# Kernel tuning notes

Measured on AMD Instinct MI355X. Metric: run time of the kernel, lower is better.

## Reference

```python
import jax, jax.numpy as jnp
import numpy as np

N = 200000
E = 6400000


def setup_inputs() -> dict:
    key = jax.random.key(0)
    k1, k2, k3, k4 = jax.random.split(key, 4)
    x = jax.random.normal(k1, (N, 10), dtype=jnp.float32)
    edge_index = jax.random.randint(k2, (2, E), 0, N, dtype=jnp.int64)
    W1 = jax.random.normal(k3, (10, 16), dtype=jnp.float32) * (1.0 / np.sqrt(10))
    b1 = jnp.zeros((16,), dtype=jnp.float32)
    W2 = jax.random.normal(k4, (16, 2), dtype=jnp.float32) * (1.0 / np.sqrt(16))
    b2 = jnp.zeros((2,), dtype=jnp.float32)
    return {"x": x, "edge_index": edge_index, "W1": W1, "b1": b1, "W2": W2, "b2": b2}


def gcn_layer(x, src, dst, W, b, num_nodes):
    # GCNConv: out = D^{-1/2} (A + I) D^{-1/2} (x W) + b, deg computed on A+I
    loop = jnp.arange(num_nodes, dtype=src.dtype)
    s = jnp.concatenate([src, loop])
    d = jnp.concatenate([dst, loop])
    deg = jax.ops.segment_sum(jnp.ones(s.shape[0], dtype=x.dtype), d, num_segments=num_nodes)
    dinv = jnp.where(deg > 0, jax.lax.rsqrt(deg), 0.0)
    norm = dinv[s] * dinv[d]                      # [E+N]
    h = x @ W                                     # [N, out] (transform before gather)
    msg = h[s] * norm[:, None]                    # [E+N, out]
    return jax.ops.segment_sum(msg, d, num_segments=num_nodes) + b


def reference(x, edge_index, W1, b1, W2, b2):
    src, dst = edge_index[0], edge_index[1]
    n = x.shape[0]
    h = jax.nn.relu(gcn_layer(x, src, dst, W1, b1, n))
    return gcn_layer(h, src, dst, W2, b2, n)
```

## Files before the change

### kernel.cpp

```cpp
#include <hip/hip_runtime.h>
#include <hip/hip_fp16.h>

#define BLK 256
#define BBLK 512
#define ABLK 512
#define DBLK 512
#define NBK 782
#define BW 256
#define CAP 8960
#define NCH 3
#define CHUNK 6144


__global__ void k_hist(const int* __restrict__ dst, int e, int* __restrict__ gcnt,
                       int* __restrict__ blockhist) {
  __shared__ int h[NBK];
  for (int i = threadIdx.x; i < NBK; i += BLK) h[i] = 0;
  __syncthreads();
  int base = blockIdx.x * CHUNK;
  int m = min(CHUNK, e - base);
  for (int k = threadIdx.x; k < m; k += BLK) atomicAdd(&h[dst[base + k] >> 8], 1);
  __syncthreads();
  int* row = blockhist + (size_t)blockIdx.x * NBK;
  int sft = (blockIdx.x * 193) % NBK;
  for (int bb = threadIdx.x; bb < NBK; bb += BLK) {
    int b = bb + sft; if (b >= NBK) b -= NBK;
    int c = h[b];
    row[b] = c;
    if (c) atomicAdd(&gcnt[b], c);
  }
}

__global__ void k_scan(const int* __restrict__ gcnt, int* __restrict__ gbase,
                       int* __restrict__ gcur, int e) {
  __shared__ int s[1024];
  int t = threadIdx.x;
  int v = (t < NBK) ? gcnt[t] : 0;
  s[t] = v;
  __syncthreads();
  for (int d = 1; d < 1024; d <<= 1) {
    int u = (t >= d) ? s[t - d] : 0;
    __syncthreads();
    s[t] += u;
    __syncthreads();
  }
  if (t < NBK) { int ex = s[t] - v; gbase[t] = ex; gcur[t] = ex; }
  if (t == 0) gbase[NBK] = e;
}

__global__ void __launch_bounds__(BBLK) k_bin(const int* __restrict__ src,
                                              const int* __restrict__ dst, int e,
                                              int* __restrict__ gcur,
                                              const int* __restrict__ blockhist,
                                              unsigned* __restrict__ binned) {
  __shared__ int lcnt[NBK];
  __shared__ int loff[NBK + 1];
  __shared__ int lbase[NBK];
  __shared__ int part[BBLK];
  __shared__ unsigned sorted[CHUNK];
  __shared__ unsigned short bkt16[CHUNK];
  int t = threadIdx.x;
  int base = blockIdx.x * CHUNK;
  int m = min(CHUNK, e - base);

  const int* row = blockhist + (size_t)blockIdx.x * NBK;
  for (int i = t; i < NBK; i += BBLK) lcnt[i] = row[i];
  __syncthreads();
  int b0 = 2 * t;
  int s0 = (b0 + 0 < NBK) ? lcnt[b0 + 0] : 0;
  int s1 = (b0 + 1 < NBK) ? lcnt[b0 + 1] : 0;
  int tsum = s0 + s1;
  part[t] = tsum;
  __syncthreads();
  for (int d = 1; d < BBLK; d <<= 1) {
    int u = (t >= d) ? part[t - d] : 0;
    __syncthreads();
    part[t] += u;
    __syncthreads();
  }
  int ex = part[t] - tsum;
  if (b0 + 0 < NBK) loff[b0 + 0] = ex;
  if (b0 + 1 < NBK) loff[b0 + 1] = ex + s0;
  if (t == 0) loff[NBK] = m;
  __syncthreads();
  int sft = (blockIdx.x * 193) % NBK;
  for (int bb = t; bb < NBK; bb += BBLK) {
    int b = bb + sft; if (b >= NBK) b -= NBK;
    int c = lcnt[b];
    lbase[b] = c ? atomicAdd(&gcur[b], c) : 0;
  }
  __syncthreads();
  for (int b = t; b < NBK; b += BBLK) lcnt[b] = loff[b];
  __syncthreads();
  for (int k = t; k < m; k += BBLK) {
    int d = dst[base + k];
    int b = d >> 8;
    int dl = d & 255;
    int pos = atomicAdd(&lcnt[b], 1);
    sorted[pos] = (unsigned)src[base + k] | ((unsigned)dl << 18);
    bkt16[pos] = (unsigned short)b;
  }
  __syncthreads();
  for (int i = t; i < m; i += BBLK) {
    int b = bkt16[i];
    binned[lbase[b] + (i - loff[b])] = sorted[i];
  }
}

__global__ void __launch_bounds__(DBLK) k_ldeg_t1(const unsigned* __restrict__ binned,
                                                  const int* __restrict__ gbase,
                                                  const float* __restrict__ x,
                                                  const float* __restrict__ W1,
                                                  int* __restrict__ deg,
                                                  float* __restrict__ dinv,
                                                  __half* __restrict__ hs1, int n) {
  __shared__ int cnt[2][BW];
  __shared__ float w[160];
  int t = threadIdx.x;
  cnt[t >> 8][t & 255] = 0;
  if (t < 160) w[t] = W1[t];
  __syncthreads();
  int b = blockIdx.x;
  int p0 = gbase[b], p1 = gbase[b + 1];
  int h = t >> 8;
  for (int p = p0 + t; p < p1; p += DBLK) atomicAdd(&cnt[h][binned[p] >> 18], 1);
  __syncthreads();
  if (t >= BW) return;
  int v = b * BW + t;
  int dg = cnt[0][t] + cnt[1][t];
  deg[v] = dg;
  if (v >= n) return;
  float di = rsqrtf((float)dg + 1.0f);
  dinv[v] = di;
  float xi[10];
#pragma unroll
  for (int k = 0; k < 10; k++) xi[k] = x[(size_t)v * 10 + k];
  __half2 hv[8];
#pragma unroll
  for (int j = 0; j < 8; j++) {
    float acc0 = 0.f, acc1 = 0.f;
#pragma unroll
    for (int k = 0; k < 10; k++) {
      acc0 = fmaf(xi[k], w[k * 16 + 2 * j], acc0);
      acc1 = fmaf(xi[k], w[k * 16 + 2 * j + 1], acc1);
    }
    hv[j] = __floats2half2_rn(acc0 * di, acc1 * di);
  }
  float4* o = (float4*)(hs1 + (size_t)v * 16);
  o[0] = *(float4*)&hv[0];
  o[1] = *(float4*)&hv[4];
}

__global__ void __launch_bounds__(ABLK) k_agg1s(unsigned* __restrict__ binned,
                                                const int* __restrict__ gbase,
                                                const int* __restrict__ deg,
                                                int* __restrict__ doff,
                                                const __half* __restrict__ hs1,
                                                const float* __restrict__ dinv,
                                                const float* __restrict__ b1,
                                                const float* __restrict__ W2,
                                                float* __restrict__ hs2, int n) {
  __shared__ int cnt[BW];
  __shared__ int stmp[BW];
  __shared__ int off[BW + 1];
  __shared__ int cur[BW];
  __shared__ int sorted[CAP];
  __shared__ float w2[32];
  __shared__ float sb1[16];
  int t = threadIdx.x;
  if (t < 32) w2[t] = W2[t];
  if (t >= 32 && t < 48) sb1[t - 32] = b1[t - 32];
  int bkt = blockIdx.x;
  int p0 = gbase[bkt], p1 = gbase[bkt + 1];
  const bool fast = (p1 - p0) <= CAP;
  const int j = t >> 1;
  const int c = t & 1;
  float acc[8];
#pragma unroll
  for (int q = 0; q < 8; q++) acc[q] = 0.f;

#define ACCR(R) { const __half2* h2_ = (const __half2*)&R; \
    float2 f0_ = __half22float2(h2_[0]); \
    float2 f1_ = __half22float2(h2_[1]); \
    float2 f2_ = __half22float2(h2_[2]); \
    float2 f3_ = __half22float2(h2_[3]); \
    acc[0] += f0_.x; acc[1] += f0_.y; acc[2] += f1_.x; acc[3] += f1_.y; \
    acc[4] += f2_.x; acc[5] += f2_.y; acc[6] += f3_.x; acc[7] += f3_.y; }

  int p = p0;
  int cidx = 0;
  while (p < p1) {
    int m = min(CAP, p1 - p);
    if (fast) {
      if (t < BW) cnt[t] = deg[(bkt << 8) + t];
    } else {
      if (t < BW) cnt[t] = 0;
      __syncthreads();
      for (int i = t; i < m; i += ABLK) atomicAdd(&cnt[binned[p + i] >> 18], 1);
    }
    __syncthreads();
    if (t < BW) stmp[t] = cnt[t];
    __syncthreads();
    for (int d = 1; d < BW; d <<= 1) {
      int u = 0;
      if (t < BW && t >= d) u = stmp[t - d];
      __syncthreads();
      if (t < BW) stmp[t] += u;
      __syncthreads();
    }
    if (t < BW) { int ex = stmp[t] - cnt[t]; off[t] = ex; cur[t] = ex; }
    if (t == 0) off[BW] = m;
    __syncthreads();
    for (int i = t; i < m; i += ABLK) {
      unsigned pk = binned[p + i];
      int pos = atomicAdd(&cur[pk >> 18], 1);
      sorted[pos] = (int)(pk & 0x3FFFF);
    }
    __syncthreads();
    for (int i = t; i < m; i += ABLK) binned[p + i] = (unsigned)sorted[i];
    if (cidx < NCH && t <= BW) doff[((size_t)bkt * NCH + cidx) * (BW + 1) + t] = off[t];
    int i0 = off[j], i1 = off[j + 1];
    int i = i0;
    for (; i + 3 < i1; i += 4) {
      int s0 = sorted[i + 0];
      int s1 = sorted[i + 1];
      int s2 = sorted[i + 2];
      int s3 = sorted[i + 3];
      float4 r0 = *(const float4*)(hs1 + (size_t)s0 * 16 + c * 8);
      float4 r1 = *(const float4*)(hs1 + (size_t)s1 * 16 + c * 8);
      float4 r2 = *(const float4*)(hs1 + (size_t)s2 * 16 + c * 8);
      float4 r3 = *(const float4*)(hs1 + (size_t)s3 * 16 + c * 8);
      ACCR(r0); ACCR(r1); ACCR(r2); ACCR(r3);
    }
    for (; i < i1; i++) {
      int s = sorted[i];
      float4 r = *(const float4*)(hs1 + (size_t)s * 16 + c * 8);
      ACCR(r);
    }
    __syncthreads();
    p += m;
    cidx++;
  }
#undef ACCR

  int v = bkt * BW + j;
  if (v < n) {
    float di = dinv[v];
    float4 sf = *(const float4*)(hs1 + (size_t)v * 16 + c * 8);
    const __half2* sh = (const __half2*)&sf;
    float h0c = 0.f, h1c = 0.f;
#pragma unroll
    for (int q = 0; q < 4; q++) {
      float2 sv = __half22float2(sh[q]);
      int f0 = c * 8 + 2 * q;
      int f1 = f0 + 1;
      float a0 = fmaxf(fmaf(di, acc[2 * q + 0] + sv.x, sb1[f0]), 0.f);
      float a1 = fmaxf(fmaf(di, acc[2 * q + 1] + sv.y, sb1[f1]), 0.f);
      h0c = fmaf(a0, w2[f0 * 2 + 0], fmaf(a1, w2[f1 * 2 + 0], h0c));
      h1c = fmaf(a0, w2[f0 * 2 + 1], fmaf(a1, w2[f1 * 2 + 1], h1c));
    }
    float h0 = h0c + __shfl_xor(h0c, 1);
    float h1 = h1c + __shfl_xor(h1c, 1);
    if (c == 0) {
      hs2[(size_t)v * 2 + 0] = h0 * di;
      hs2[(size_t)v * 2 + 1] = h1 * di;
    }
  }
}

__global__ void __launch_bounds__(BBLK) k_agg2(const unsigned* __restrict__ binned,
                                               const int* __restrict__ gbase,
                                               const int* __restrict__ doff,
                                               const float* __restrict__ hs2,
                                               const float* __restrict__ dinv,
                                               const float* __restrict__ b2,
                                               float* __restrict__ out, int n) {
  int t = threadIdx.x;
  int j = t >> 1;
  int c = t & 1;
  int bkt = blockIdx.x;
  int p0 = gbase[bkt], p1 = gbase[bkt + 1];
  float a0 = 0.f, a1 = 0.f;
  int cidx = 0;
  for (int p = p0; p < p1; p += CAP, cidx++) {
    const int* row = doff + ((size_t)bkt * NCH + cidx) * (BW + 1);
    int i0 = row[j], i1 = row[j + 1];
    const unsigned* bp = binned + p;
    int i = i0 + c;
    for (; i + 6 < i1; i += 8) {
      int s0 = bp[i + 0];
      int s1 = bp[i + 2];
      int s2 = bp[i + 4];
      int s3 = bp[i + 6];
      float2 m0 = *(const float2*)(hs2 + (size_t)s0 * 2);
      float2 m1 = *(const float2*)(hs2 + (size_t)s1 * 2);
      float2 m2 = *(const float2*)(hs2 + (size_t)s2 * 2);
      float2 m3 = *(const float2*)(hs2 + (size_t)s3 * 2);
      a0 += m0.x + m1.x + m2.x + m3.x;
      a1 += m0.y + m1.y + m2.y + m3.y;
    }
    for (; i < i1; i += 2) {
      float2 m = *(const float2*)(hs2 + (size_t)bp[i] * 2);
      a0 += m.x;
      a1 += m.y;
    }
  }
  a0 += __shfl_xor(a0, 1);
  a1 += __shfl_xor(a1, 1);
  int v = bkt * BW + j;
  if (c == 0 && v < n) {
    float di = dinv[v];
    out[(size_t)v * 2 + 0] = fmaf(di, a0 + hs2[(size_t)v * 2 + 0], b2[0]);
    out[(size_t)v * 2 + 1] = fmaf(di, a1 + hs2[(size_t)v * 2 + 1], b2[1]);
  }
}

extern "C" void kernel_launch(void* const* d_in, const int* in_sizes, int n_in,
                              void* d_out, int out_size, void* d_ws, size_t ws_size,
                              hipStream_t stream) {
  const float* x  = (const float*)d_in[0];
  const int*   ei = (const int*)d_in[1];
  const float* W1 = (const float*)d_in[2];
  const float* b1 = (const float*)d_in[3];
  const float* W2 = (const float*)d_in[4];
  const float* b2 = (const float*)d_in[5];
  float* out = (float*)d_out;

  const int n = in_sizes[0] / 10;
  const int e = in_sizes[1] / 2;
  const int* src = ei;
  const int* dst = ei + e;

  int gC = (e + CHUNK - 1) / CHUNK;

  char* ws = (char*)d_ws;
  int*      gcnt      = (int*)ws;      ws += (size_t)NBK * 4;
  int*      gbase     = (int*)ws;      ws += ((size_t)NBK + 1) * 4;
  int*      gcur      = (int*)ws;      ws += (size_t)NBK * 4;
  int*      deg       = (int*)ws;      ws += (size_t)NBK * BW * 4;
  int*      doff      = (int*)ws;      ws += (size_t)NBK * NCH * (BW + 1) * 4;
  int*      blockhist = (int*)ws;      ws += (size_t)gC * NBK * 4;
  unsigned* binned    = (unsigned*)ws; ws += (size_t)e * 4;
  float*    dinv      = (float*)ws;    ws += (size_t)n * 4;
  __half*   hs1       = (__half*)ws;   ws += (size_t)n * 16 * 2;
  float*    hs2       = (float*)ws;    ws += (size_t)n * 2 * 4;

  hipMemsetAsync(gcnt, 0, (size_t)NBK * 4, stream);
  k_hist<<<gC, BLK, 0, stream>>>(dst, e, gcnt, blockhist);
  k_scan<<<1, 1024, 0, stream>>>(gcnt, gbase, gcur, e);
  k_bin<<<gC, BBLK, 0, stream>>>(src, dst, e, gcur, blockhist, binned);
  k_ldeg_t1<<<NBK, DBLK, 0, stream>>>(binned, gbase, x, W1, deg, dinv, hs1, n);
  k_agg1s<<<NBK, ABLK, 0, stream>>>(binned, gbase, deg, doff, hs1, dinv, b1, W2, hs2, n);
  k_agg2<<<NBK, BBLK, 0, stream>>>(binned, gbase, doff, hs2, dinv, b2, out, n);
}
```

Baseline: 320.1 us.

## Split half-precision features into two planes and add nontemporal streaming loads

Stores the 16-channel fp16 layer-1 features as two separate 8-channel planes, each 16 bytes per node. The aggregation kernel now makes two passes over the edge list, one per plane, with the two lanes of a pair splitting the edges between them, then combines the partial sums with shuffles. This halves the working set of each gather pass, aiming for better cache hit rates on the random gathers. It also marks the streaming reads and writes of edge indices, histograms and binned data as nontemporal, so they pollute the cache less. The cost is an extra pass over the sorted edge list and extra shuffles.

```diff
diff --git a/kernel.cpp b/kernel.cpp
--- a/kernel.cpp
+++ b/kernel.cpp
@@ -7,6 +7,7 @@
 #define DBLK 512
 #define NBK 782
 #define BW 256
+#define NPAD (NBK * BW)
 #define CAP 8960
 #define NCH 3
 #define CHUNK 6144
@@ -19,14 +20,15 @@
   __syncthreads();
   int base = blockIdx.x * CHUNK;
   int m = min(CHUNK, e - base);
-  for (int k = threadIdx.x; k < m; k += BLK) atomicAdd(&h[dst[base + k] >> 8], 1);
+  for (int k = threadIdx.x; k < m; k += BLK)
+    atomicAdd(&h[__builtin_nontemporal_load(&dst[base + k]) >> 8], 1);
   __syncthreads();
   int* row = blockhist + (size_t)blockIdx.x * NBK;
   int sft = (blockIdx.x * 193) % NBK;
   for (int bb = threadIdx.x; bb < NBK; bb += BLK) {
     int b = bb + sft; if (b >= NBK) b -= NBK;
     int c = h[b];
-    row[b] = c;
+    __builtin_nontemporal_store(c, &row[b]);
     if (c) atomicAdd(&gcnt[b], c);
   }
 }
@@ -64,7 +66,7 @@
   int m = min(CHUNK, e - base);
 
   const int* row = blockhist + (size_t)blockIdx.x * NBK;
-  for (int i = t; i < NBK; i += BBLK) lcnt[i] = row[i];
+  for (int i = t; i < NBK; i += BBLK) lcnt[i] = __builtin_nontemporal_load(&row[i]);
   __syncthreads();
   int b0 = 2 * t;
   int s0 = (b0 + 0 < NBK) ? lcnt[b0 + 0] : 0;
@@ -93,17 +95,17 @@
   for (int b = t; b < NBK; b += BBLK) lcnt[b] = loff[b];
   __syncthreads();
   for (int k = t; k < m; k += BBLK) {
-    int d = dst[base + k];
+    int d = __builtin_nontemporal_load(&dst[base + k]);
     int b = d >> 8;
     int dl = d & 255;
     int pos = atomicAdd(&lcnt[b], 1);
-    sorted[pos] = (unsigned)src[base + k] | ((unsigned)dl << 18);
+    sorted[pos] = (unsigned)__builtin_nontemporal_load(&src[base + k]) | ((unsigned)dl << 18);
     bkt16[pos] = (unsigned short)b;
   }
   __syncthreads();
   for (int i = t; i < m; i += BBLK) {
     int b = bkt16[i];
-    binned[lbase[b] + (i - loff[b])] = sorted[i];
+    __builtin_nontemporal_store(sorted[i], &binned[lbase[b] + (i - loff[b])]);
   }
 }
 
@@ -123,7 +125,8 @@
   int b = blockIdx.x;
   int p0 = gbase[b], p1 = gbase[b + 1];
   int h = t >> 8;
-  for (int p = p0 + t; p < p1; p += DBLK) atomicAdd(&cnt[h][binned[p] >> 18], 1);
+  for (int p = p0 + t; p < p1; p += DBLK)
+    atomicAdd(&cnt[h][__builtin_nontemporal_load(&binned[p]) >> 18], 1);
   __syncthreads();
   if (t >= BW) return;
   int v = b * BW + t;
@@ -146,9 +149,8 @@
     }
     hv[j] = __floats2half2_rn(acc0 * di, acc1 * di);
   }
-  float4* o = (float4*)(hs1 + (size_t)v * 16);
-  o[0] = *(float4*)&hv[0];
-  o[1] = *(float4*)&hv[4];
+  *(float4*)(hs1 + (size_t)v * 8) = *(float4*)&hv[0];
+  *(float4*)(hs1 + ((size_t)NPAD + v) * 8) = *(float4*)&hv[4];
 }
 
 __global__ void __launch_bounds__(ABLK) k_agg1s(unsigned* __restrict__ binned,
@@ -175,17 +177,19 @@
   const bool fast = (p1 - p0) <= CAP;
   const int j = t >> 1;
   const int c = t & 1;
-  float acc[8];
-#pragma unroll
-  for (int q = 0; q < 8; q++) acc[q] = 0.f;
-
-#define ACCR(R) { const __half2* h2_ = (const __half2*)&R; \
+  const __half* pl0 = hs1;
+  const __half* pl1 = hs1 + (size_t)NPAD * 8;
+  float accA[8], accB[8];
+#pragma unroll
+  for (int q = 0; q < 8; q++) { accA[q] = 0.f; accB[q] = 0.f; }
+
+#define ACC8(A, R) { const __half2* h2_ = (const __half2*)&R; \
     float2 f0_ = __half22float2(h2_[0]); \
     float2 f1_ = __half22float2(h2_[1]); \
     float2 f2_ = __half22float2(h2_[2]); \
     float2 f3_ = __half22float2(h2_[3]); \
-    acc[0] += f0_.x; acc[1] += f0_.y; acc[2] += f1_.x; acc[3] += f1_.y; \
-    acc[4] += f2_.x; acc[5] += f2_.y; acc[6] += f3_.x; acc[7] += f3_.y; }
+    A[0] += f0_.x; A[1] += f0_.y; A[2] += f1_.x; A[3] += f1_.y; \
+    A[4] += f2_.x; A[5] += f2_.y; A[6] += f3_.x; A[7] += f3_.y; }
 
   int p = p0;
   int cidx = 0;
@@ -196,7 +200,8 @@
     } else {
       if (t < BW) cnt[t] = 0;
       __syncthreads();
-      for (int i = t; i < m; i += ABLK) atomicAdd(&cnt[binned[p + i] >> 18], 1);
+      for (int i = t; i < m; i += ABLK)
+        atomicAdd(&cnt[__builtin_nontemporal_load(&binned[p + i]) >> 18], 1);
     }
     __syncthreads();
     if (t < BW) stmp[t] = cnt[t];
@@ -212,41 +217,67 @@
     if (t == 0) off[BW] = m;
     __syncthreads();
     for (int i = t; i < m; i += ABLK) {
-      unsigned pk = binned[p + i];
+      unsigned pk = __builtin_nontemporal_load(&binned[p + i]);
       int pos = atomicAdd(&cur[pk >> 18], 1);
       sorted[pos] = (int)(pk & 0x3FFFF);
     }
     __syncthreads();
-    for (int i = t; i < m; i += ABLK) binned[p + i] = (unsigned)sorted[i];
+    for (int i = t; i < m; i += ABLK)
+      __builtin_nontemporal_store((unsigned)sorted[i], &binned[p + i]);
     if (cidx < NCH && t <= BW) doff[((size_t)bkt * NCH + cidx) * (BW + 1) + t] = off[t];
     int i0 = off[j], i1 = off[j + 1];
-    int i = i0;
-    for (; i + 3 < i1; i += 4) {
+    int i = i0 + c;
+    for (; i + 6 < i1; i += 8) {
       int s0 = sorted[i + 0];
-      int s1 = sorted[i + 1];
-      int s2 = sorted[i + 2];
-      int s3 = sorted[i + 3];
-      float4 r0 = *(const float4*)(hs1 + (size_t)s0 * 16 + c * 8);
-      float4 r1 = *(const float4*)(hs1 + (size_t)s1 * 16 + c * 8);
-      float4 r2 = *(const float4*)(hs1 + (size_t)s2 * 16 + c * 8);
-      float4 r3 = *(const float4*)(hs1 + (size_t)s3 * 16 + c * 8);
-      ACCR(r0); ACCR(r1); ACCR(r2); ACCR(r3);
-    }
-    for (; i < i1; i++) {
-      int s = sorted[i];
-      float4 r = *(const float4*)(hs1 + (size_t)s * 16 + c * 8);
-      ACCR(r);
+      int s1 = sorted[i + 2];
+      int s2 = sorted[i + 4];
+      int s3 = sorted[i + 6];
+      float4 r0 = *(const float4*)(pl0 + (size_t)s0 * 8);
+      float4 r1 = *(const float4*)(pl0 + (size_t)s1 * 8);
+      float4 r2 = *(const float4*)(pl0 + (size_t)s2 * 8);
+      float4 r3 = *(const float4*)(pl0 + (size_t)s3 * 8);
+      ACC8(accA, r0); ACC8(accA, r1); ACC8(accA, r2); ACC8(accA, r3);
+    }
+    for (; i < i1; i += 2) {
+      float4 r = *(const float4*)(pl0 + (size_t)sorted[i] * 8);
+      ACC8(accA, r);
+    }
+    __syncthreads();
+    i = i0 + c;
+    for (; i + 6 < i1; i += 8) {
+      int s0 = sorted[i + 0];
+      int s1 = sorted[i + 2];
+      int s2 = sorted[i + 4];
+      int s3 = sorted[i + 6];
+      float4 r0 = *(const float4*)(pl1 + (size_t)s0 * 8);
+      float4 r1 = *(const float4*)(pl1 + (size_t)s1 * 8);
+      float4 r2 = *(const float4*)(pl1 + (size_t)s2 * 8);
+      float4 r3 = *(const float4*)(pl1 + (size_t)s3 * 8);
+      ACC8(accB, r0); ACC8(accB, r1); ACC8(accB, r2); ACC8(accB, r3);
+    }
+    for (; i < i1; i += 2) {
+      float4 r = *(const float4*)(pl1 + (size_t)sorted[i] * 8);
+      ACC8(accB, r);
     }
     __syncthreads();
     p += m;
     cidx++;
   }
-#undef ACCR
+#undef ACC8
+
+  float acc[8];
+#pragma unroll
+  for (int q = 0; q < 8; q++) {
+    accA[q] += __shfl_xor(accA[q], 1);
+    accB[q] += __shfl_xor(accB[q], 1);
+    acc[q] = c ? accB[q] : accA[q];
+  }
 
   int v = bkt * BW + j;
   if (v < n) {
     float di = dinv[v];
-    float4 sf = *(const float4*)(hs1 + (size_t)v * 16 + c * 8);
+    const __half* plc = c ? pl1 : pl0;
+    float4 sf = *(const float4*)(plc + (size_t)v * 8);
     const __half2* sh = (const __half2*)&sf;
     float h0c = 0.f, h1c = 0.f;
 #pragma unroll
@@ -288,10 +319,10 @@
     const unsigned* bp = binned + p;
     int i = i0 + c;
     for (; i + 6 < i1; i += 8) {
-      int s0 = bp[i + 0];
-      int s1 = bp[i + 2];
-      int s2 = bp[i + 4];
-      int s3 = bp[i + 6];
+      int s0 = __builtin_nontemporal_load(&bp[i + 0]);
+      int s1 = __builtin_nontemporal_load(&bp[i + 2]);
+      int s2 = __builtin_nontemporal_load(&bp[i + 4]);
+      int s3 = __builtin_nontemporal_load(&bp[i + 6]);
       float2 m0 = *(const float2*)(hs2 + (size_t)s0 * 2);
       float2 m1 = *(const float2*)(hs2 + (size_t)s1 * 2);
       float2 m2 = *(const float2*)(hs2 + (size_t)s2 * 2);
@@ -300,7 +331,7 @@
       a1 += m0.y + m1.y + m2.y + m3.y;
     }
     for (; i < i1; i += 2) {
-      float2 m = *(const float2*)(hs2 + (size_t)bp[i] * 2);
+      float2 m = *(const float2*)(hs2 + (size_t)__builtin_nontemporal_load(&bp[i]) * 2);
       a0 += m.x;
       a1 += m.y;
     }
@@ -337,12 +368,12 @@
   int*      gcnt      = (int*)ws;      ws += (size_t)NBK * 4;
   int*      gbase     = (int*)ws;      ws += ((size_t)NBK + 1) * 4;
   int*      gcur      = (int*)ws;      ws += (size_t)NBK * 4;
-  int*      deg       = (int*)ws;      ws += (size_t)NBK * BW * 4;
+  int*      deg       = (int*)ws;      ws += (size_t)NPAD * 4;
   int*      doff      = (int*)ws;      ws += (size_t)NBK * NCH * (BW + 1) * 4;
   int*      blockhist = (int*)ws;      ws += (size_t)gC * NBK * 4;
   unsigned* binned    = (unsigned*)ws; ws += (size_t)e * 4;
   float*    dinv      = (float*)ws;    ws += (size_t)n * 4;
-  __half*   hs1       = (__half*)ws;   ws += (size_t)n * 16 * 2;
+  __half*   hs1       = (__half*)ws;   ws += (size_t)NPAD * 16 * 2;
   float*    hs2       = (float*)ws;    ws += (size_t)n * 2 * 4;
 
   hipMemsetAsync(gcnt, 0, (size_t)NBK * 4, stream);
```

New measurement: 400.1 us. 25.0% more time.

## Split per-node edge lists by source half and add nontemporal loads/stores

Applied to the files above, without the earlier changes.

The layer-1 aggregation now sorts each bucket's edges by destination node and then by which half of the node range the source falls in. All threads process their low-half sources first, hit a block barrier, and then process the high-half sources, so the gather working set in hs1 at any moment stays smaller and more cache-friendly. The degree histogram becomes a 512-key histogram to support this split. Streaming reads and writes of the edge arrays, block histograms and binned lists are also switched to nontemporal builtins so they pollute the cache less. The extra barrier and the larger scan add synchronisation overhead, and hs1 is padded to the full bucket range.

```diff
diff --git a/kernel.cpp b/kernel.cpp
--- a/kernel.cpp
+++ b/kernel.cpp
@@ -7,6 +7,9 @@
 #define DBLK 512
 #define NBK 782
 #define BW 256
+#define NK2 512
+#define NPAD (NBK * BW)
+#define HALF (NPAD / 2)
 #define CAP 8960
 #define NCH 3
 #define CHUNK 6144
@@ -19,14 +22,15 @@
   __syncthreads();
   int base = blockIdx.x * CHUNK;
   int m = min(CHUNK, e - base);
-  for (int k = threadIdx.x; k < m; k += BLK) atomicAdd(&h[dst[base + k] >> 8], 1);
+  for (int k = threadIdx.x; k < m; k += BLK)
+    atomicAdd(&h[__builtin_nontemporal_load(&dst[base + k]) >> 8], 1);
   __syncthreads();
   int* row = blockhist + (size_t)blockIdx.x * NBK;
   int sft = (blockIdx.x * 193) % NBK;
   for (int bb = threadIdx.x; bb < NBK; bb += BLK) {
     int b = bb + sft; if (b >= NBK) b -= NBK;
     int c = h[b];
-    row[b] = c;
+    __builtin_nontemporal_store(c, &row[b]);
     if (c) atomicAdd(&gcnt[b], c);
   }
 }
@@ -64,7 +68,7 @@
   int m = min(CHUNK, e - base);
 
   const int* row = blockhist + (size_t)blockIdx.x * NBK;
-  for (int i = t; i < NBK; i += BBLK) lcnt[i] = row[i];
+  for (int i = t; i < NBK; i += BBLK) lcnt[i] = __builtin_nontemporal_load(&row[i]);
   __syncthreads();
   int b0 = 2 * t;
   int s0 = (b0 + 0 < NBK) ? lcnt[b0 + 0] : 0;
@@ -93,17 +97,17 @@
   for (int b = t; b < NBK; b += BBLK) lcnt[b] = loff[b];
   __syncthreads();
   for (int k = t; k < m; k += BBLK) {
-    int d = dst[base + k];
+    int d = __builtin_nontemporal_load(&dst[base + k]);
     int b = d >> 8;
     int dl = d & 255;
     int pos = atomicAdd(&lcnt[b], 1);
-    sorted[pos] = (unsigned)src[base + k] | ((unsigned)dl << 18);
+    sorted[pos] = (unsigned)__builtin_nontemporal_load(&src[base + k]) | ((unsigned)dl << 18);
     bkt16[pos] = (unsigned short)b;
   }
   __syncthreads();
   for (int i = t; i < m; i += BBLK) {
     int b = bkt16[i];
-    binned[lbase[b] + (i - loff[b])] = sorted[i];
+    __builtin_nontemporal_store(sorted[i], &binned[lbase[b] + (i - loff[b])]);
   }
 }
 
@@ -111,25 +115,30 @@
                                                   const int* __restrict__ gbase,
                                                   const float* __restrict__ x,
                                                   const float* __restrict__ W1,
-                                                  int* __restrict__ deg,
+                                                  int* __restrict__ deg2,
                                                   float* __restrict__ dinv,
                                                   __half* __restrict__ hs1, int n) {
-  __shared__ int cnt[2][BW];
+  __shared__ int cnt[2][NK2];
   __shared__ float w[160];
   int t = threadIdx.x;
-  cnt[t >> 8][t & 255] = 0;
+  cnt[0][t] = 0;
+  cnt[1][t] = 0;
   if (t < 160) w[t] = W1[t];
   __syncthreads();
   int b = blockIdx.x;
   int p0 = gbase[b], p1 = gbase[b + 1];
   int h = t >> 8;
-  for (int p = p0 + t; p < p1; p += DBLK) atomicAdd(&cnt[h][binned[p] >> 18], 1);
-  __syncthreads();
+  for (int p = p0 + t; p < p1; p += DBLK) {
+    unsigned u = __builtin_nontemporal_load(&binned[p]);
+    int key = (int)((u >> 18) << 1) | (int)((u & 0x3FFFFu) >= HALF);
+    atomicAdd(&cnt[h][key], 1);
+  }
+  __syncthreads();
+  deg2[(size_t)b * NK2 + t] = cnt[0][t] + cnt[1][t];
   if (t >= BW) return;
   int v = b * BW + t;
-  int dg = cnt[0][t] + cnt[1][t];
-  deg[v] = dg;
   if (v >= n) return;
+  int dg = cnt[0][2 * t] + cnt[0][2 * t + 1] + cnt[1][2 * t] + cnt[1][2 * t + 1];
   float di = rsqrtf((float)dg + 1.0f);
   dinv[v] = di;
   float xi[10];
@@ -153,17 +162,15 @@
 
 __global__ void __launch_bounds__(ABLK) k_agg1s(unsigned* __restrict__ binned,
                                                 const int* __restrict__ gbase,
-                                                const int* __restrict__ deg,
+                                                const int* __restrict__ deg2,
                                                 int* __restrict__ doff,
                                                 const __half* __restrict__ hs1,
                                                 const float* __restrict__ dinv,
                                                 const float* __restrict__ b1,
                                                 const float* __restrict__ W2,
                                                 float* __restrict__ hs2, int n) {
-  __shared__ int cnt[BW];
-  __shared__ int stmp[BW];
-  __shared__ int off[BW + 1];
-  __shared__ int cur[BW];
+  __shared__ int cnt[NK2];
+  __shared__ int off[NK2 + 1];
   __shared__ int sorted[CAP];
   __shared__ float w2[32];
   __shared__ float sb1[16];
@@ -192,36 +199,43 @@
   while (p < p1) {
     int m = min(CAP, p1 - p);
     if (fast) {
-      if (t < BW) cnt[t] = deg[(bkt << 8) + t];
+      cnt[t] = deg2[(size_t)bkt * NK2 + t];
     } else {
-      if (t < BW) cnt[t] = 0;
+      cnt[t] = 0;
       __syncthreads();
-      for (int i = t; i < m; i += ABLK) atomicAdd(&cnt[binned[p + i] >> 18], 1);
-    }
-    __syncthreads();
-    if (t < BW) stmp[t] = cnt[t];
-    __syncthreads();
-    for (int d = 1; d < BW; d <<= 1) {
-      int u = 0;
-      if (t < BW && t >= d) u = stmp[t - d];
+      for (int i = t; i < m; i += ABLK) {
+        unsigned u = __builtin_nontemporal_load(&binned[p + i]);
+        int key = (int)((u >> 18) << 1) | (int)((u & 0x3FFFFu) >= HALF);
+        atomicAdd(&cnt[key], 1);
+      }
+    }
+    __syncthreads();
+    int myv = cnt[t];
+    for (int d = 1; d < NK2; d <<= 1) {
+      int u = (t >= d) ? cnt[t - d] : 0;
       __syncthreads();
-      if (t < BW) stmp[t] += u;
+      cnt[t] += u;
       __syncthreads();
     }
-    if (t < BW) { int ex = stmp[t] - cnt[t]; off[t] = ex; cur[t] = ex; }
-    if (t == 0) off[BW] = m;
+    off[t] = cnt[t] - myv;
+    if (t == 0) off[NK2] = m;
+    __syncthreads();
+    cnt[t] = off[t];
     __syncthreads();
     for (int i = t; i < m; i += ABLK) {
-      unsigned pk = binned[p + i];
-      int pos = atomicAdd(&cur[pk >> 18], 1);
-      sorted[pos] = (int)(pk & 0x3FFFF);
-    }
-    __syncthreads();
-    for (int i = t; i < m; i += ABLK) binned[p + i] = (unsigned)sorted[i];
-    if (cidx < NCH && t <= BW) doff[((size_t)bkt * NCH + cidx) * (BW + 1) + t] = off[t];
-    int i0 = off[j], i1 = off[j + 1];
-    int i = i0;
-    for (; i + 3 < i1; i += 4) {
+      unsigned pk = __builtin_nontemporal_load(&binned[p + i]);
+      int srcv = (int)(pk & 0x3FFFFu);
+      int key = (int)((pk >> 18) << 1) | (int)(srcv >= HALF);
+      int pos = atomicAdd(&cnt[key], 1);
+      sorted[pos] = srcv;
+    }
+    __syncthreads();
+    for (int i = t; i < m; i += ABLK)
+      __builtin_nontemporal_store((unsigned)sorted[i], &binned[p + i]);
+    if (cidx < NCH && t <= BW) doff[((size_t)bkt * NCH + cidx) * (BW + 1) + t] = off[2 * t];
+    int iA0 = off[2 * j], iA1 = off[2 * j + 1], iB1 = off[2 * j + 2];
+    int i = iA0;
+    for (; i + 3 < iA1; i += 4) {
       int s0 = sorted[i + 0];
       int s1 = sorted[i + 1];
       int s2 = sorted[i + 2];
@@ -232,9 +246,24 @@
       float4 r3 = *(const float4*)(hs1 + (size_t)s3 * 16 + c * 8);
       ACCR(r0); ACCR(r1); ACCR(r2); ACCR(r3);
     }
-    for (; i < i1; i++) {
-      int s = sorted[i];
-      float4 r = *(const float4*)(hs1 + (size_t)s * 16 + c * 8);
+    for (; i < iA1; i++) {
+      float4 r = *(const float4*)(hs1 + (size_t)sorted[i] * 16 + c * 8);
+      ACCR(r);
+    }
+    __syncthreads();
+    for (; i + 3 < iB1; i += 4) {
+      int s0 = sorted[i + 0];
+      int s1 = sorted[i + 1];
+      int s2 = sorted[i + 2];
+      int s3 = sorted[i + 3];
+      float4 r0 = *(const float4*)(hs1 + (size_t)s0 * 16 + c * 8);
+      float4 r1 = *(const float4*)(hs1 + (size_t)s1 * 16 + c * 8);
+      float4 r2 = *(const float4*)(hs1 + (size_t)s2 * 16 + c * 8);
+      float4 r3 = *(const float4*)(hs1 + (size_t)s3 * 16 + c * 8);
+      ACCR(r0); ACCR(r1); ACCR(r2); ACCR(r3);
+    }
+    for (; i < iB1; i++) {
+      float4 r = *(const float4*)(hs1 + (size_t)sorted[i] * 16 + c * 8);
       ACCR(r);
     }
     __syncthreads();
@@ -288,10 +317,10 @@
     const unsigned* bp = binned + p;
     int i = i0 + c;
     for (; i + 6 < i1; i += 8) {
-      int s0 = bp[i + 0];
-      int s1 = bp[i + 2];
-      int s2 = bp[i + 4];
-      int s3 = bp[i + 6];
+      int s0 = __builtin_nontemporal_load(&bp[i + 0]);
+      int s1 = __builtin_nontemporal_load(&bp[i + 2]);
+      int s2 = __builtin_nontemporal_load(&bp[i + 4]);
+      int s3 = __builtin_nontemporal_load(&bp[i + 6]);
       float2 m0 = *(const float2*)(hs2 + (size_t)s0 * 2);
       float2 m1 = *(const float2*)(hs2 + (size_t)s1 * 2);
       float2 m2 = *(const float2*)(hs2 + (size_t)s2 * 2);
@@ -300,7 +329,7 @@
       a1 += m0.y + m1.y + m2.y + m3.y;
     }
     for (; i < i1; i += 2) {
-      float2 m = *(const float2*)(hs2 + (size_t)bp[i] * 2);
+      float2 m = *(const float2*)(hs2 + (size_t)__builtin_nontemporal_load(&bp[i]) * 2);
       a0 += m.x;
       a1 += m.y;
     }
@@ -337,19 +366,19 @@
   int*      gcnt      = (int*)ws;      ws += (size_t)NBK * 4;
   int*      gbase     = (int*)ws;      ws += ((size_t)NBK + 1) * 4;
   int*      gcur      = (int*)ws;      ws += (size_t)NBK * 4;
-  int*      deg       = (int*)ws;      ws += (size_t)NBK * BW * 4;
+  int*      deg2      = (int*)ws;      ws += (size_t)NBK * NK2 * 4;
   int*      doff      = (int*)ws;      ws += (size_t)NBK * NCH * (BW + 1) * 4;
   int*      blockhist = (int*)ws;      ws += (size_t)gC * NBK * 4;
   unsigned* binned    = (unsigned*)ws; ws += (size_t)e * 4;
   float*    dinv      = (float*)ws;    ws += (size_t)n * 4;
-  __half*   hs1       = (__half*)ws;   ws += (size_t)n * 16 * 2;
+  __half*   hs1       = (__half*)ws;   ws += (size_t)NPAD * 16 * 2;
   float*    hs2       = (float*)ws;    ws += (size_t)n * 2 * 4;
 
   hipMemsetAsync(gcnt, 0, (size_t)NBK * 4, stream);
   k_hist<<<gC, BLK, 0, stream>>>(dst, e, gcnt, blockhist);
   k_scan<<<1, 1024, 0, stream>>>(gcnt, gbase, gcur, e);
   k_bin<<<gC, BBLK, 0, stream>>>(src, dst, e, gcur, blockhist, binned);
-  k_ldeg_t1<<<NBK, DBLK, 0, stream>>>(binned, gbase, x, W1, deg, dinv, hs1, n);
-  k_agg1s<<<NBK, ABLK, 0, stream>>>(binned, gbase, deg, doff, hs1, dinv, b1, W2, hs2, n);
+  k_ldeg_t1<<<NBK, DBLK, 0, stream>>>(binned, gbase, x, W1, deg2, dinv, hs1, n);
+  k_agg1s<<<NBK, ABLK, 0, stream>>>(binned, gbase, deg2, doff, hs1, dinv, b1, W2, hs2, n);
   k_agg2<<<NBK, BBLK, 0, stream>>>(binned, gbase, doff, hs2, dinv, b2, out, n);
 }
```

Measured after the change: 378.7 us. 1.18x slower.
